# Kernel optimization log

Hardware: AMD Instinct MI355X
Metric: run time of the kernel (lower is better)

The kernel has to match this reference:

```python
import jax, jax.numpy as jnp
import numpy as np

EMSIZE = 1024
NHEAD = 16
HEAD = EMSIZE // NHEAD


def setup_inputs() -> dict:
    key = jax.random.key(0)
    ks = jax.random.split(key, 8)
    s = 1.0 / np.sqrt(EMSIZE)
    return {
        "embed": jax.random.normal(ks[0], (2, 2048, EMSIZE), dtype=jnp.float32),
        "q": jax.random.normal(ks[1], (2, 2048, EMSIZE), dtype=jnp.float32),
        "Wk": jax.random.normal(ks[2], (EMSIZE, EMSIZE), dtype=jnp.float32) * s,
        "bk": jnp.zeros((EMSIZE,), dtype=jnp.float32),
        "Wq": jax.random.normal(ks[3], (EMSIZE, EMSIZE), dtype=jnp.float32) * s,
        "bq": jnp.zeros((EMSIZE,), dtype=jnp.float32),
        "Wv": jax.random.normal(ks[4], (EMSIZE, EMSIZE), dtype=jnp.float32) * s,
        "bv": jnp.zeros((EMSIZE,), dtype=jnp.float32),
    }


def _split_heads(x):
    # [b, s, E] -> [b, h, s, d]
    b, s, _ = x.shape
    return x.reshape(b, s, NHEAD, HEAD).transpose(0, 2, 1, 3)


def reference(embed, q, Wk, bk, Wq, bq, Wv, bv):
    # torch Linear: y = x @ W.T + b
    k = _split_heads(embed @ Wk.T + bk)   # [b, h, skv, d]
    qh = _split_heads(q @ Wq.T + bq)      # [b, h, sq, d]
    v = _split_heads(embed @ Wv.T + bv)   # [b, h, skv, d]
    scale = 1.0 / np.sqrt(HEAD).astype(np.float32)
    scores = jnp.einsum("bhqd,bhkd->bhqk", qh, k) * scale
    attn = jax.nn.softmax(scores, axis=-1)  # dropout p=0 -> identity
    ctx = jnp.einsum("bhqk,bhkd->bhqd", attn, v)
    b, h, sq, d = ctx.shape
    return ctx.transpose(0, 2, 1, 3).reshape(b, sq, h * d)
```

## Files before the change

### kernel.cpp

```cpp
#include <hip/hip_runtime.h>
#include <cstdint>
#include <cstddef>


using bf16 = __bf16;
typedef __bf16 bf16x8 __attribute__((ext_vector_type(8)));
typedef float f32x4 __attribute__((ext_vector_type(4)));
typedef float f32x16 __attribute__((ext_vector_type(16)));
using uint32 = unsigned int;

__device__ __forceinline__ void async16(void* lds, const void* g) {
  __builtin_amdgcn_global_load_lds((__attribute__((address_space(1))) void*)g,
                                   (__attribute__((address_space(3))) void*)lds,
                                   16, 0, 0);
}

__device__ __forceinline__ uint32 pack_bf16x2(float lo, float hi_) {
  union { bf16 h[2]; uint32 u; } w;
  w.h[0] = (bf16)lo; w.h[1] = (bf16)hi_;
  return w.u;
}

__global__ void cast_all_kernel(const float* __restrict__ e, const float* __restrict__ q,
                                const float* __restrict__ wk, const float* __restrict__ wq,
                                const float* __restrict__ wv, bf16* __restrict__ dst) {
  int i = blockIdx.x * blockDim.x + threadIdx.x;
  if (i >= 2883584) return;
  const float* src; int off;
  if (i < 1048576)      { src = e;  off = 0; }
  else if (i < 2097152) { src = q;  off = 1048576; }
  else if (i < 2359296) { src = wk; off = 2097152; }
  else if (i < 2621440) { src = wq; off = 2359296; }
  else                  { src = wv; off = 2621440; }
  float4 v = reinterpret_cast<const float4*>(src)[i - off];
  union { bf16 h[4]; unsigned long long u; } o;
  o.h[0] = (bf16)v.x; o.h[1] = (bf16)v.y; o.h[2] = (bf16)v.z; o.h[3] = (bf16)v.w;
  reinterpret_cast<unsigned long long*>(dst)[i] = o.u;
}

__global__ __launch_bounds__(256) void proj_kernel(
    const bf16* __restrict__ emb, const bf16* __restrict__ qin,
    const bf16* __restrict__ wk, const bf16* __restrict__ wq, const bf16* __restrict__ wv,
    const float* __restrict__ bk, const float* __restrict__ bq, const float* __restrict__ bv,
    bf16* __restrict__ Kp, bf16* __restrict__ Qp, bf16* __restrict__ Vt)
{
  __shared__ bf16 As[128 * 64];
  __shared__ bf16 Bs[128 * 64];

  int pid = blockIdx.x;
  int proj = pid >> 8;
  int t = pid & 255;
  int m0 = (t >> 3) * 128;
  int n0 = (t & 7) * 128;

  const bf16* A = (proj == 1) ? qin : emb;
  const bf16* W = (proj == 0) ? wk : (proj == 1) ? wq : wv;
  const float* bias = (proj == 0) ? bk : (proj == 1) ? bq : bv;
  const bool proj2 = (proj == 2);

  int tid = threadIdx.x;
  int lane = tid & 63, wid = tid >> 6;
  int quad = lane >> 4, l16 = lane & 15;
  int moff = (wid & 1) * 64, noff = (wid >> 1) * 64;

  f32x4 zero = {0.f, 0.f, 0.f, 0.f};
  f32x4 acc[4][4];
#pragma unroll
  for (int i = 0; i < 4; i++)
#pragma unroll
    for (int j = 0; j < 4; j++) acc[i][j] = zero;

  for (int kk = 0; kk < 1024; kk += 64) {
    __syncthreads();
#pragma unroll
    for (int i = 0; i < 4; i++) {
      int c = i * 256 + tid;
      int row = c >> 3;
      int ko = ((c ^ row) & 7) << 3;
      async16(&As[(size_t)(i * 256 + wid * 64) * 8], &A[(size_t)(m0 + row) * 1024 + kk + ko]);
      async16(&Bs[(size_t)(i * 256 + wid * 64) * 8], &W[(size_t)(n0 + row) * 1024 + kk + ko]);
    }
    __syncthreads();
#pragma unroll
    for (int ks = 0; ks < 2; ks++) {
      bf16x8 af[4], bfr[4];
#pragma unroll
      for (int i = 0; i < 4; i++) {
        int row = moff + i * 16 + l16;
        af[i] = *reinterpret_cast<const bf16x8*>(&As[row * 64 + ((((ks << 2) | quad) ^ row) & 7) * 8]);
      }
#pragma unroll
      for (int j = 0; j < 4; j++) {
        int row = noff + j * 16 + l16;
        bfr[j] = *reinterpret_cast<const bf16x8*>(&Bs[row * 64 + ((((ks << 2) | quad) ^ row) & 7) * 8]);
      }
      if (proj2) {
#pragma unroll
        for (int i = 0; i < 4; i++)
#pragma unroll
          for (int j = 0; j < 4; j++)
            acc[i][j] = __builtin_amdgcn_mfma_f32_16x16x32_bf16(bfr[j], af[i], acc[i][j], 0, 0, 0);
      } else {
#pragma unroll
        for (int i = 0; i < 4; i++)
#pragma unroll
          for (int j = 0; j < 4; j++)
            acc[i][j] = __builtin_amdgcn_mfma_f32_16x16x32_bf16(af[i], bfr[j], acc[i][j], 0, 0, 0);
      }
    }
  }

  if (proj2) {
#pragma unroll
    for (int i = 0; i < 4; i++) {
      int grow = m0 + moff + i * 16 + l16;
      int bb = grow >> 11;
      int ss = grow & 2047;
#pragma unroll
      for (int j = 0; j < 4; j++) {
#pragma unroll
        for (int r = 0; r < 4; r++) {
          int gcol = n0 + noff + j * 16 + quad * 4 + r;
          int hh = gcol >> 6, dd = gcol & 63;
          int bh = bb * 16 + hh;
          float v = acc[i][j][r] + bias[gcol];
          Vt[((size_t)bh * 64 + dd) * 2048 + ss] = (bf16)v;
        }
      }
    }
  } else {
    float bvv[4];
#pragma unroll
    for (int j = 0; j < 4; j++) bvv[j] = bias[n0 + noff + j * 16 + l16];
    bf16* dst = (proj == 0) ? Kp : Qp;
    const float qs = (proj == 1) ? 0.18033688011112042f : 1.0f;
#pragma unroll
    for (int i = 0; i < 4; i++) {
#pragma unroll
      for (int r = 0; r < 4; r++) {
        int grow = m0 + moff + i * 16 + quad * 4 + r;
        int bb = grow >> 11;
        int ss = grow & 2047;
#pragma unroll
        for (int j = 0; j < 4; j++) {
          int gcol = n0 + noff + j * 16 + l16;
          int hh = gcol >> 6, dd = gcol & 63;
          int bh = bb * 16 + hh;
          float v = (acc[i][j][r] + bvv[j]) * qs;
          dst[((size_t)bh * 2048 + ss) * 64 + dd] = (bf16)v;
        }
      }
    }
  }
}

__global__ __launch_bounds__(256, 2) void attn_kernel(
    const bf16* __restrict__ Qp, const bf16* __restrict__ Kp, const bf16* __restrict__ Vt,
    float* __restrict__ out, float* __restrict__ part1, float* __restrict__ lbuf)
{
  __shared__ bf16 Ks[2][64 * 64];
  __shared__ bf16 Vs[2][64 * 64];

  int bid = blockIdx.x;
  int half = bid & 1;
  int q0 = ((bid >> 1) & 7) << 8;
  int bh = bid >> 4;
  int bb = bh >> 4, hh = bh & 15;
  int g0 = half << 4;

  const bf16* Qg = Qp + (size_t)bh * (2048 * 64);
  const bf16* Kg = Kp + (size_t)bh * (2048 * 64);
  const bf16* Vg = Vt + (size_t)bh * (64 * 2048);

  int tid = threadIdx.x, lane = tid & 63, wid = tid >> 6;
  int l32 = lane & 31;
  int h = lane >> 5;
  int wq0 = q0 + wid * 64;

  auto stage = [&](int kt_, int buf) {
#pragma unroll
    for (int i = 0; i < 2; i++) {
      int c = i * 256 + tid;
      int row = c >> 3;
      int srow = (row & ~12) | ((row & 4) << 1) | ((row & 8) >> 1);
      int ko = ((c ^ row) & 7) << 3;
      async16(&Ks[buf][(size_t)(i * 256 + wid * 64) * 8], &Kg[(size_t)(kt_ * 64 + srow) * 64 + ko]);
      async16(&Vs[buf][(size_t)(i * 256 + wid * 64) * 8], &Vg[(size_t)row * 2048 + kt_ * 64 + ko]);
    }
  };

  bf16x8 qf[2][4];
#pragma unroll
  for (int u = 0; u < 2; u++)
#pragma unroll
    for (int s = 0; s < 4; s++)
      qf[u][s] = *reinterpret_cast<const bf16x8*>(
          &Qg[(size_t)(wq0 + u * 32 + l32) * 64 + s * 16 + h * 8]);

  stage(g0, 0);

  const f32x16 z16 = {0.f, 0.f, 0.f, 0.f, 0.f, 0.f, 0.f, 0.f,
                      0.f, 0.f, 0.f, 0.f, 0.f, 0.f, 0.f, 0.f};
  f32x16 Ov[2][2];
  Ov[0][0] = z16; Ov[0][1] = z16; Ov[1][0] = z16; Ov[1][1] = z16;
  float l_i[2] = {0.f, 0.f};

  for (int kt = 0; kt < 16; kt++) {
    int cur = kt & 1;
    __syncthreads();
    __builtin_amdgcn_sched_barrier(0);
    if (kt < 15) stage(g0 + kt + 1, cur ^ 1);
    __builtin_amdgcn_sched_barrier(0);

    const bf16* Kc = Ks[cur];
    const bf16* Vc = Vs[cur];

#pragma unroll
    for (int t = 0; t < 2; t++) {
      f32x16 St[2];
      int row = t * 32 + l32;
      {
        bf16x8 kf = *reinterpret_cast<const bf16x8*>(&Kc[row * 64 + ((h ^ row) & 7) * 8]);
        St[0] = __builtin_amdgcn_mfma_f32_32x32x16_bf16(kf, qf[0][0], z16, 0, 0, 0);
        St[1] = __builtin_amdgcn_mfma_f32_32x32x16_bf16(kf, qf[1][0], z16, 0, 0, 0);
      }
#pragma unroll
      for (int s = 1; s < 4; s++) {
        int j8 = s * 2 + h;
        bf16x8 kf = *reinterpret_cast<const bf16x8*>(&Kc[row * 64 + ((j8 ^ row) & 7) * 8]);
        St[0] = __builtin_amdgcn_mfma_f32_32x32x16_bf16(kf, qf[0][s], St[0], 0, 0, 0);
        St[1] = __builtin_amdgcn_mfma_f32_32x32x16_bf16(kf, qf[1][s], St[1], 0, 0, 0);
      }

      uint32 pk[2][8];
#pragma unroll
      for (int u = 0; u < 2; u++) {
#pragma unroll
        for (int i = 0; i < 16; i++) {
          float p = __builtin_amdgcn_exp2f(St[u][i]);
          St[u][i] = p;
          l_i[u] += p;
        }
#pragma unroll
        for (int i = 0; i < 8; i++)
          pk[u][i] = pack_bf16x2(St[u][2 * i], St[u][2 * i + 1]);
      }

#pragma unroll
      for (int g = 0; g < 2; g++) {
        union { uint32 u[4]; bf16x8 v; } pb0, pb1;
#pragma unroll
        for (int i = 0; i < 4; i++) { pb0.u[i] = pk[0][g * 4 + i]; pb1.u[i] = pk[1][g * 4 + i]; }
        int j8 = t * 4 + g * 2 + h;
#pragma unroll
        for (int dt = 0; dt < 2; dt++) {
          int rowv = dt * 32 + l32;
          bf16x8 vf = *reinterpret_cast<const bf16x8*>(&Vc[rowv * 64 + ((j8 ^ rowv) & 7) * 8]);
          Ov[0][dt] = __builtin_amdgcn_mfma_f32_32x32x16_bf16(vf, pb0.v, Ov[0][dt], 0, 0, 0);
          Ov[1][dt] = __builtin_amdgcn_mfma_f32_32x32x16_bf16(vf, pb1.v, Ov[1][dt], 0, 0, 0);
        }
      }
    }
  }

#pragma unroll
  for (int u = 0; u < 2; u++) {
    float l_tot = l_i[u] + __shfl_xor(l_i[u], 32);
    int q = wq0 + u * 32 + l32;
    float* dstO = (half == 0 ? out : part1) + ((size_t)bb * 2048 + q) * 1024 + hh * 64;
#pragma unroll
    for (int dt = 0; dt < 2; dt++)
#pragma unroll
      for (int g = 0; g < 4; g++) {
        float4 o;
        o.x = Ov[u][dt][4 * g + 0];
        o.y = Ov[u][dt][4 * g + 1];
        o.z = Ov[u][dt][4 * g + 2];
        o.w = Ov[u][dt][4 * g + 3];
        *reinterpret_cast<float4*>(&dstO[dt * 32 + g * 8 + 4 * h]) = o;
      }
    if (h == 0) lbuf[half * 65536 + (bh << 11) + q] = l_tot;
  }
}

__global__ __launch_bounds__(256) void combine_kernel(
    float* __restrict__ out, const float* __restrict__ part1,
    const float* __restrict__ lbuf) {
  int i = blockIdx.x * 256 + threadIdx.x;
  int e = i << 2;
  int brow = e >> 10;
  int b = brow >> 11;
  int hcol = (e >> 6) & 15;
  int srow = brow & 2047;
  int lidx = ((b * 16 + hcol) << 11) + srow;
  float inv = 1.0f / (lbuf[lidx] + lbuf[65536 + lidx]);
  float4 a = reinterpret_cast<const float4*>(out)[i];
  float4 p = reinterpret_cast<const float4*>(part1)[i];
  float4 r;
  r.x = (a.x + p.x) * inv;
  r.y = (a.y + p.y) * inv;
  r.z = (a.z + p.z) * inv;
  r.w = (a.w + p.w) * inv;
  reinterpret_cast<float4*>(out)[i] = r;
}

extern "C" void kernel_launch(void* const* d_in, const int* in_sizes, int n_in,
                              void* d_out, int out_size, void* d_ws, size_t ws_size,
                              hipStream_t stream) {
  (void)in_sizes; (void)n_in; (void)out_size; (void)ws_size;
  const float* embed = (const float*)d_in[0];
  const float* qin   = (const float*)d_in[1];
  const float* Wk    = (const float*)d_in[2];
  const float* bk    = (const float*)d_in[3];
  const float* Wq    = (const float*)d_in[4];
  const float* bq    = (const float*)d_in[5];
  const float* Wv    = (const float*)d_in[6];
  const float* bv    = (const float*)d_in[7];
  float* out = (float*)d_out;

  bf16* ws = (bf16*)d_ws;
  bf16* emb_bf = ws;
  bf16* q_bf   = emb_bf + 4194304;
  bf16* wk_bf  = q_bf   + 4194304;
  bf16* wq_bf  = wk_bf  + 1048576;
  bf16* wv_bf  = wq_bf  + 1048576;
  bf16* Kp     = wv_bf  + 1048576;
  bf16* Qp     = Kp     + 4194304;
  bf16* Vt     = Qp     + 4194304;

  float* part1 = (float*)d_ws;
  float* lbuf  = part1 + 4194304;

  cast_all_kernel<<<11264, 256, 0, stream>>>(embed, qin, Wk, Wq, Wv, ws);

  proj_kernel<<<768, 256, 0, stream>>>(emb_bf, q_bf, wk_bf, wq_bf, wv_bf,
                                       bk, bq, bv, Kp, Qp, Vt);
  attn_kernel<<<512, 256, 0, stream>>>(Qp, Kp, Vt, out, part1, lbuf);
  combine_kernel<<<4096, 256, 0, stream>>>(out, part1, lbuf);
}
```

Baseline: 193.6 us.

## Restructure attention inner loop: batch K loads, compute all QK scores, prioritize MFMA phases

Reorders the per-tile attention loop so that all K fragments are loaded from LDS first and both QK^T score blocks are computed back to back. V fragments are then loaded ahead of each softmax/PV phase. s_setprio raises wave priority around the MFMA bursts so that different waves' matrix and exp work interleave better. The row-sum accumulator is split into two independent partial sums to shorten the dependency chain. In exchange, more fragments are held in registers at once (all K fragments plus both score tiles), which raises VGPR pressure and may lower occupancy.

```diff
diff --git a/kernel.cpp b/kernel.cpp
--- a/kernel.cpp
+++ b/kernel.cpp
@@ -203,7 +203,8 @@
                       0.f, 0.f, 0.f, 0.f, 0.f, 0.f, 0.f, 0.f};
   f32x16 Ov[2][2];
   Ov[0][0] = z16; Ov[0][1] = z16; Ov[1][0] = z16; Ov[1][1] = z16;
-  float l_i[2] = {0.f, 0.f};
+  float2 l2[2];
+  l2[0].x = 0.f; l2[0].y = 0.f; l2[1].x = 0.f; l2[1].y = 0.f;
 
   for (int kt = 0; kt < 16; kt++) {
     int cur = kt & 1;
@@ -215,57 +216,110 @@
     const bf16* Kc = Ks[cur];
     const bf16* Vc = Vs[cur];
 
+    bf16x8 kf[2][4];
 #pragma unroll
     for (int t = 0; t < 2; t++) {
-      f32x16 St[2];
       int row = t * 32 + l32;
-      {
-        bf16x8 kf = *reinterpret_cast<const bf16x8*>(&Kc[row * 64 + ((h ^ row) & 7) * 8]);
-        St[0] = __builtin_amdgcn_mfma_f32_32x32x16_bf16(kf, qf[0][0], z16, 0, 0, 0);
-        St[1] = __builtin_amdgcn_mfma_f32_32x32x16_bf16(kf, qf[1][0], z16, 0, 0, 0);
-      }
+#pragma unroll
+      for (int s = 0; s < 4; s++) {
+        int j8 = s * 2 + h;
+        kf[t][s] = *reinterpret_cast<const bf16x8*>(&Kc[row * 64 + ((j8 ^ row) & 7) * 8]);
+      }
+    }
+
+    f32x16 St[2][2];
+    __builtin_amdgcn_s_setprio(1);
+#pragma unroll
+    for (int t = 0; t < 2; t++) {
+      St[t][0] = __builtin_amdgcn_mfma_f32_32x32x16_bf16(kf[t][0], qf[0][0], z16, 0, 0, 0);
+      St[t][1] = __builtin_amdgcn_mfma_f32_32x32x16_bf16(kf[t][0], qf[1][0], z16, 0, 0, 0);
 #pragma unroll
       for (int s = 1; s < 4; s++) {
-        int j8 = s * 2 + h;
-        bf16x8 kf = *reinterpret_cast<const bf16x8*>(&Kc[row * 64 + ((j8 ^ row) & 7) * 8]);
-        St[0] = __builtin_amdgcn_mfma_f32_32x32x16_bf16(kf, qf[0][s], St[0], 0, 0, 0);
-        St[1] = __builtin_amdgcn_mfma_f32_32x32x16_bf16(kf, qf[1][s], St[1], 0, 0, 0);
-      }
-
-      uint32 pk[2][8];
-#pragma unroll
-      for (int u = 0; u < 2; u++) {
-#pragma unroll
-        for (int i = 0; i < 16; i++) {
-          float p = __builtin_amdgcn_exp2f(St[u][i]);
-          St[u][i] = p;
-          l_i[u] += p;
-        }
-#pragma unroll
-        for (int i = 0; i < 8; i++)
-          pk[u][i] = pack_bf16x2(St[u][2 * i], St[u][2 * i + 1]);
-      }
-
-#pragma unroll
-      for (int g = 0; g < 2; g++) {
-        union { uint32 u[4]; bf16x8 v; } pb0, pb1;
-#pragma unroll
-        for (int i = 0; i < 4; i++) { pb0.u[i] = pk[0][g * 4 + i]; pb1.u[i] = pk[1][g * 4 + i]; }
-        int j8 = t * 4 + g * 2 + h;
-#pragma unroll
-        for (int dt = 0; dt < 2; dt++) {
-          int rowv = dt * 32 + l32;
-          bf16x8 vf = *reinterpret_cast<const bf16x8*>(&Vc[rowv * 64 + ((j8 ^ rowv) & 7) * 8]);
-          Ov[0][dt] = __builtin_amdgcn_mfma_f32_32x32x16_bf16(vf, pb0.v, Ov[0][dt], 0, 0, 0);
-          Ov[1][dt] = __builtin_amdgcn_mfma_f32_32x32x16_bf16(vf, pb1.v, Ov[1][dt], 0, 0, 0);
-        }
-      }
-    }
+        St[t][0] = __builtin_amdgcn_mfma_f32_32x32x16_bf16(kf[t][s], qf[0][s], St[t][0], 0, 0, 0);
+        St[t][1] = __builtin_amdgcn_mfma_f32_32x32x16_bf16(kf[t][s], qf[1][s], St[t][1], 0, 0, 0);
+      }
+    }
+    __builtin_amdgcn_s_setprio(0);
+
+    bf16x8 vf0[2][2];
+#pragma unroll
+    for (int g = 0; g < 2; g++) {
+      int j8 = g * 2 + h;
+#pragma unroll
+      for (int dt = 0; dt < 2; dt++) {
+        int rowv = dt * 32 + l32;
+        vf0[g][dt] = *reinterpret_cast<const bf16x8*>(&Vc[rowv * 64 + ((j8 ^ rowv) & 7) * 8]);
+      }
+    }
+
+    uint32 pk0[2][8];
+#pragma unroll
+    for (int u = 0; u < 2; u++) {
+#pragma unroll
+      for (int i = 0; i < 8; i++) {
+        float pe = __builtin_amdgcn_exp2f(St[0][u][2 * i]);
+        float po = __builtin_amdgcn_exp2f(St[0][u][2 * i + 1]);
+        l2[u].x += pe; l2[u].y += po;
+        pk0[u][i] = pack_bf16x2(pe, po);
+      }
+    }
+
+    __builtin_amdgcn_s_setprio(1);
+#pragma unroll
+    for (int g = 0; g < 2; g++) {
+      union { uint32 u[4]; bf16x8 v; } pb0, pb1;
+#pragma unroll
+      for (int i = 0; i < 4; i++) { pb0.u[i] = pk0[0][g * 4 + i]; pb1.u[i] = pk0[1][g * 4 + i]; }
+#pragma unroll
+      for (int dt = 0; dt < 2; dt++) {
+        Ov[0][dt] = __builtin_amdgcn_mfma_f32_32x32x16_bf16(vf0[g][dt], pb0.v, Ov[0][dt], 0, 0, 0);
+        Ov[1][dt] = __builtin_amdgcn_mfma_f32_32x32x16_bf16(vf0[g][dt], pb1.v, Ov[1][dt], 0, 0, 0);
+      }
+    }
+    __builtin_amdgcn_s_setprio(0);
+
+    bf16x8 vf1[2][2];
+#pragma unroll
+    for (int g = 0; g < 2; g++) {
+      int j8 = 4 + g * 2 + h;
+#pragma unroll
+      for (int dt = 0; dt < 2; dt++) {
+        int rowv = dt * 32 + l32;
+        vf1[g][dt] = *reinterpret_cast<const bf16x8*>(&Vc[rowv * 64 + ((j8 ^ rowv) & 7) * 8]);
+      }
+    }
+
+    uint32 pk1[2][8];
+#pragma unroll
+    for (int u = 0; u < 2; u++) {
+#pragma unroll
+      for (int i = 0; i < 8; i++) {
+        float pe = __builtin_amdgcn_exp2f(St[1][u][2 * i]);
+        float po = __builtin_amdgcn_exp2f(St[1][u][2 * i + 1]);
+        l2[u].x += pe; l2[u].y += po;
+        pk1[u][i] = pack_bf16x2(pe, po);
+      }
+    }
+
+    __builtin_amdgcn_s_setprio(1);
+#pragma unroll
+    for (int g = 0; g < 2; g++) {
+      union { uint32 u[4]; bf16x8 v; } pb0, pb1;
+#pragma unroll
+      for (int i = 0; i < 4; i++) { pb0.u[i] = pk1[0][g * 4 + i]; pb1.u[i] = pk1[1][g * 4 + i]; }
+#pragma unroll
+      for (int dt = 0; dt < 2; dt++) {
+        Ov[0][dt] = __builtin_amdgcn_mfma_f32_32x32x16_bf16(vf1[g][dt], pb0.v, Ov[0][dt], 0, 0, 0);
+        Ov[1][dt] = __builtin_amdgcn_mfma_f32_32x32x16_bf16(vf1[g][dt], pb1.v, Ov[1][dt], 0, 0, 0);
+      }
+    }
+    __builtin_amdgcn_s_setprio(0);
   }
 
 #pragma unroll
   for (int u = 0; u < 2; u++) {
-    float l_tot = l_i[u] + __shfl_xor(l_i[u], 32);
+    float l_half = l2[u].x + l2[u].y;
+    float l_tot = l_half + __shfl_xor(l_half, 32);
     int q = wq0 + u * 32 + l32;
     float* dstO = (half == 0 ? out : part1) + ((size_t)bb * 2048 + q) * 1024 + hh * 64;
 #pragma unroll
```

Result: no change. 196.2 us (+1.3%).

## Split attention work across 8 waves with 32 query rows each

Applied to the files above, without the earlier changes.

The attention kernel now launches 512 threads per block, and each wave handles 32 query rows instead of 64. This halves the per-wave accumulators and Q fragments so more waves can be resident (launch bounds 512,4). K/V staging now takes one async load per thread instead of two. Each K/V fragment read from LDS now feeds one MFMA instead of two, so there is less register-level reuse and more LDS traffic per MFMA.

```diff
diff --git a/kernel.cpp b/kernel.cpp
--- a/kernel.cpp
+++ b/kernel.cpp
@@ -154,7 +154,7 @@
   }
 }
 
-__global__ __launch_bounds__(256, 2) void attn_kernel(
+__global__ __launch_bounds__(512, 4) void attn_kernel(
     const bf16* __restrict__ Qp, const bf16* __restrict__ Kp, const bf16* __restrict__ Vt,
     float* __restrict__ out, float* __restrict__ part1, float* __restrict__ lbuf)
 {
@@ -175,35 +175,31 @@
   int tid = threadIdx.x, lane = tid & 63, wid = tid >> 6;
   int l32 = lane & 31;
   int h = lane >> 5;
-  int wq0 = q0 + wid * 64;
+  int wq0 = q0 + wid * 32;
 
   auto stage = [&](int kt_, int buf) {
-#pragma unroll
-    for (int i = 0; i < 2; i++) {
-      int c = i * 256 + tid;
-      int row = c >> 3;
-      int srow = (row & ~12) | ((row & 4) << 1) | ((row & 8) >> 1);
-      int ko = ((c ^ row) & 7) << 3;
-      async16(&Ks[buf][(size_t)(i * 256 + wid * 64) * 8], &Kg[(size_t)(kt_ * 64 + srow) * 64 + ko]);
-      async16(&Vs[buf][(size_t)(i * 256 + wid * 64) * 8], &Vg[(size_t)row * 2048 + kt_ * 64 + ko]);
-    }
+    int c = tid;
+    int row = c >> 3;
+    int srow = (row & ~12) | ((row & 4) << 1) | ((row & 8) >> 1);
+    int ko = ((c ^ row) & 7) << 3;
+    async16(&Ks[buf][(size_t)(wid * 64) * 8], &Kg[(size_t)(kt_ * 64 + srow) * 64 + ko]);
+    async16(&Vs[buf][(size_t)(wid * 64) * 8], &Vg[(size_t)row * 2048 + kt_ * 64 + ko]);
   };
 
-  bf16x8 qf[2][4];
-#pragma unroll
-  for (int u = 0; u < 2; u++)
-#pragma unroll
-    for (int s = 0; s < 4; s++)
-      qf[u][s] = *reinterpret_cast<const bf16x8*>(
-          &Qg[(size_t)(wq0 + u * 32 + l32) * 64 + s * 16 + h * 8]);
+  bf16x8 qf[4];
+#pragma unroll
+  for (int s = 0; s < 4; s++)
+    qf[s] = *reinterpret_cast<const bf16x8*>(
+        &Qg[(size_t)(wq0 + l32) * 64 + s * 16 + h * 8]);
 
   stage(g0, 0);
 
   const f32x16 z16 = {0.f, 0.f, 0.f, 0.f, 0.f, 0.f, 0.f, 0.f,
                       0.f, 0.f, 0.f, 0.f, 0.f, 0.f, 0.f, 0.f};
-  f32x16 Ov[2][2];
-  Ov[0][0] = z16; Ov[0][1] = z16; Ov[1][0] = z16; Ov[1][1] = z16;
-  float l_i[2] = {0.f, 0.f};
+  f32x16 Ov[2];
+  Ov[0] = z16; Ov[1] = z16;
+  float2 l2;
+  l2.x = 0.f; l2.y = 0.f;
 
   for (int kt = 0; kt < 16; kt++) {
     int cur = kt & 1;
@@ -217,66 +213,58 @@
 
 #pragma unroll
     for (int t = 0; t < 2; t++) {
-      f32x16 St[2];
+      f32x16 St;
       int row = t * 32 + l32;
       {
         bf16x8 kf = *reinterpret_cast<const bf16x8*>(&Kc[row * 64 + ((h ^ row) & 7) * 8]);
-        St[0] = __builtin_amdgcn_mfma_f32_32x32x16_bf16(kf, qf[0][0], z16, 0, 0, 0);
-        St[1] = __builtin_amdgcn_mfma_f32_32x32x16_bf16(kf, qf[1][0], z16, 0, 0, 0);
+        St = __builtin_amdgcn_mfma_f32_32x32x16_bf16(kf, qf[0], z16, 0, 0, 0);
       }
 #pragma unroll
       for (int s = 1; s < 4; s++) {
         int j8 = s * 2 + h;
         bf16x8 kf = *reinterpret_cast<const bf16x8*>(&Kc[row * 64 + ((j8 ^ row) & 7) * 8]);
-        St[0] = __builtin_amdgcn_mfma_f32_32x32x16_bf16(kf, qf[0][s], St[0], 0, 0, 0);
-        St[1] = __builtin_amdgcn_mfma_f32_32x32x16_bf16(kf, qf[1][s], St[1], 0, 0, 0);
-      }
-
-      uint32 pk[2][8];
-#pragma unroll
-      for (int u = 0; u < 2; u++) {
-#pragma unroll
-        for (int i = 0; i < 16; i++) {
-          float p = __builtin_amdgcn_exp2f(St[u][i]);
-          St[u][i] = p;
-          l_i[u] += p;
-        }
-#pragma unroll
-        for (int i = 0; i < 8; i++)
-          pk[u][i] = pack_bf16x2(St[u][2 * i], St[u][2 * i + 1]);
+        St = __builtin_amdgcn_mfma_f32_32x32x16_bf16(kf, qf[s], St, 0, 0, 0);
+      }
+
+      uint32 pk[8];
+#pragma unroll
+      for (int i = 0; i < 8; i++) {
+        float pe = __builtin_amdgcn_exp2f(St[2 * i]);
+        float po = __builtin_amdgcn_exp2f(St[2 * i + 1]);
+        l2.x += pe; l2.y += po;
+        pk[i] = pack_bf16x2(pe, po);
       }
 
 #pragma unroll
       for (int g = 0; g < 2; g++) {
-        union { uint32 u[4]; bf16x8 v; } pb0, pb1;
-#pragma unroll
-        for (int i = 0; i < 4; i++) { pb0.u[i] = pk[0][g * 4 + i]; pb1.u[i] = pk[1][g * 4 + i]; }
+        union { uint32 u[4]; bf16x8 v; } pb;
+#pragma unroll
+        for (int i = 0; i < 4; i++) pb.u[i] = pk[g * 4 + i];
         int j8 = t * 4 + g * 2 + h;
 #pragma unroll
         for (int dt = 0; dt < 2; dt++) {
           int rowv = dt * 32 + l32;
           bf16x8 vf = *reinterpret_cast<const bf16x8*>(&Vc[rowv * 64 + ((j8 ^ rowv) & 7) * 8]);
-          Ov[0][dt] = __builtin_amdgcn_mfma_f32_32x32x16_bf16(vf, pb0.v, Ov[0][dt], 0, 0, 0);
-          Ov[1][dt] = __builtin_amdgcn_mfma_f32_32x32x16_bf16(vf, pb1.v, Ov[1][dt], 0, 0, 0);
+          Ov[dt] = __builtin_amdgcn_mfma_f32_32x32x16_bf16(vf, pb.v, Ov[dt], 0, 0, 0);
         }
       }
     }
   }
 
-#pragma unroll
-  for (int u = 0; u < 2; u++) {
-    float l_tot = l_i[u] + __shfl_xor(l_i[u], 32);
-    int q = wq0 + u * 32 + l32;
+  {
+    float l_half = l2.x + l2.y;
+    float l_tot = l_half + __shfl_xor(l_half, 32);
+    int q = wq0 + l32;
     float* dstO = (half == 0 ? out : part1) + ((size_t)bb * 2048 + q) * 1024 + hh * 64;
 #pragma unroll
     for (int dt = 0; dt < 2; dt++)
 #pragma unroll
       for (int g = 0; g < 4; g++) {
         float4 o;
-        o.x = Ov[u][dt][4 * g + 0];
-        o.y = Ov[u][dt][4 * g + 1];
-        o.z = Ov[u][dt][4 * g + 2];
-        o.w = Ov[u][dt][4 * g + 3];
+        o.x = Ov[dt][4 * g + 0];
+        o.y = Ov[dt][4 * g + 1];
+        o.z = Ov[dt][4 * g + 2];
+        o.w = Ov[dt][4 * g + 3];
         *reinterpret_cast<float4*>(&dstO[dt * 32 + g * 8 + 4 * h]) = o;
       }
     if (h == 0) lbuf[half * 65536 + (bh << 11) + q] = l_tot;
@@ -335,6 +323,6 @@
 
   proj_kernel<<<768, 256, 0, stream>>>(emb_bf, q_bf, wk_bf, wq_bf, wv_bf,
                                        bk, bq, bv, Kp, Qp, Vt);
-  attn_kernel<<<512, 256, 0, stream>>>(Qp, Kp, Vt, out, part1, lbuf);
+  attn_kernel<<<512, 512, 0, stream>>>(Qp, Kp, Vt, out, part1, lbuf);
   combine_kernel<<<4096, 256, 0, stream>>>(out, part1, lbuf);
 }
```

New measurement: 192.5 us. About the same (-0.6%).

## Split KV across waves within block and reduce in LDS, drop combine kernel

Applied to the files above, without the earlier changes.

The attention kernel now uses 512-thread blocks, each covering 128 query rows. Eight waves split the key sequence four ways (two 64-key tiles per stage and two 32-row halves), and the partial outputs and row sums are reduced through shared memory at the end. This removes the separate combine kernel and the global round trip of partial outputs and sums, and adds a block-index swizzle. In exchange it adds more LDS traffic and extra barriers in the epilogue, and needs more registers per block.

```diff
diff --git a/kernel.cpp b/kernel.cpp
--- a/kernel.cpp
+++ b/kernel.cpp
@@ -154,19 +154,19 @@
   }
 }
 
-__global__ __launch_bounds__(256, 2) void attn_kernel(
+__global__ __launch_bounds__(512, 4) void attn_kernel(
     const bf16* __restrict__ Qp, const bf16* __restrict__ Kp, const bf16* __restrict__ Vt,
-    float* __restrict__ out, float* __restrict__ part1, float* __restrict__ lbuf)
+    float* __restrict__ out)
 {
-  __shared__ bf16 Ks[2][64 * 64];
-  __shared__ bf16 Vs[2][64 * 64];
-
-  int bid = blockIdx.x;
-  int half = bid & 1;
-  int q0 = ((bid >> 1) & 7) << 8;
-  int bh = bid >> 4;
+  __shared__ bf16 Ks[2][2][64 * 64];
+  __shared__ bf16 Vs[2][2][64 * 64];
+  __shared__ float lsh[4][128];
+
+  int swz = (blockIdx.x & 7) * 64 + (blockIdx.x >> 3);
+  int qblk = swz & 15;
+  int bh = swz >> 4;
+  int q0 = qblk << 7;
   int bb = bh >> 4, hh = bh & 15;
-  int g0 = half << 4;
 
   const bf16* Qg = Qp + (size_t)bh * (2048 * 64);
   const bf16* Kg = Kp + (size_t)bh * (2048 * 64);
@@ -175,17 +175,21 @@
   int tid = threadIdx.x, lane = tid & 63, wid = tid >> 6;
   int l32 = lane & 31;
   int h = lane >> 5;
-  int wq0 = q0 + wid * 64;
-
-  auto stage = [&](int kt_, int buf) {
-#pragma unroll
-    for (int i = 0; i < 2; i++) {
-      int c = i * 256 + tid;
+  int qh = wid & 1;
+  int kh = (wid >> 1) & 1;
+  int ts = wid >> 2;
+  int wq0 = q0 + qh * 64;
+
+  auto stage = [&](int kp_, int buf) {
+#pragma unroll
+    for (int s = 0; s < 2; s++) {
+      int kt_ = kp_ * 2 + s;
+      int c = tid;
       int row = c >> 3;
       int srow = (row & ~12) | ((row & 4) << 1) | ((row & 8) >> 1);
       int ko = ((c ^ row) & 7) << 3;
-      async16(&Ks[buf][(size_t)(i * 256 + wid * 64) * 8], &Kg[(size_t)(kt_ * 64 + srow) * 64 + ko]);
-      async16(&Vs[buf][(size_t)(i * 256 + wid * 64) * 8], &Vg[(size_t)row * 2048 + kt_ * 64 + ko]);
+      async16(&Ks[buf][s][(size_t)wid * 512], &Kg[(size_t)(kt_ * 64 + srow) * 64 + ko]);
+      async16(&Vs[buf][s][(size_t)wid * 512], &Vg[(size_t)row * 2048 + kt_ * 64 + ko]);
     }
   };
 
@@ -197,111 +201,165 @@
       qf[u][s] = *reinterpret_cast<const bf16x8*>(
           &Qg[(size_t)(wq0 + u * 32 + l32) * 64 + s * 16 + h * 8]);
 
-  stage(g0, 0);
+  stage(0, 0);
 
   const f32x16 z16 = {0.f, 0.f, 0.f, 0.f, 0.f, 0.f, 0.f, 0.f,
                       0.f, 0.f, 0.f, 0.f, 0.f, 0.f, 0.f, 0.f};
   f32x16 Ov[2][2];
   Ov[0][0] = z16; Ov[0][1] = z16; Ov[1][0] = z16; Ov[1][1] = z16;
-  float l_i[2] = {0.f, 0.f};
-
-  for (int kt = 0; kt < 16; kt++) {
-    int cur = kt & 1;
+  float2 l2[2];
+  l2[0].x = 0.f; l2[0].y = 0.f; l2[1].x = 0.f; l2[1].y = 0.f;
+
+  int row = kh * 32 + l32;
+
+  for (int kp = 0; kp < 16; kp++) {
+    int cur = kp & 1;
     __syncthreads();
     __builtin_amdgcn_sched_barrier(0);
-    if (kt < 15) stage(g0 + kt + 1, cur ^ 1);
+    if (kp < 15) stage(kp + 1, cur ^ 1);
     __builtin_amdgcn_sched_barrier(0);
 
-    const bf16* Kc = Ks[cur];
-    const bf16* Vc = Vs[cur];
-
-#pragma unroll
-    for (int t = 0; t < 2; t++) {
-      f32x16 St[2];
-      int row = t * 32 + l32;
-      {
-        bf16x8 kf = *reinterpret_cast<const bf16x8*>(&Kc[row * 64 + ((h ^ row) & 7) * 8]);
-        St[0] = __builtin_amdgcn_mfma_f32_32x32x16_bf16(kf, qf[0][0], z16, 0, 0, 0);
-        St[1] = __builtin_amdgcn_mfma_f32_32x32x16_bf16(kf, qf[1][0], z16, 0, 0, 0);
-      }
-#pragma unroll
-      for (int s = 1; s < 4; s++) {
-        int j8 = s * 2 + h;
-        bf16x8 kf = *reinterpret_cast<const bf16x8*>(&Kc[row * 64 + ((j8 ^ row) & 7) * 8]);
-        St[0] = __builtin_amdgcn_mfma_f32_32x32x16_bf16(kf, qf[0][s], St[0], 0, 0, 0);
-        St[1] = __builtin_amdgcn_mfma_f32_32x32x16_bf16(kf, qf[1][s], St[1], 0, 0, 0);
-      }
-
-      uint32 pk[2][8];
-#pragma unroll
-      for (int u = 0; u < 2; u++) {
-#pragma unroll
-        for (int i = 0; i < 16; i++) {
-          float p = __builtin_amdgcn_exp2f(St[u][i]);
-          St[u][i] = p;
-          l_i[u] += p;
-        }
-#pragma unroll
-        for (int i = 0; i < 8; i++)
-          pk[u][i] = pack_bf16x2(St[u][2 * i], St[u][2 * i + 1]);
-      }
-
-#pragma unroll
-      for (int g = 0; g < 2; g++) {
-        union { uint32 u[4]; bf16x8 v; } pb0, pb1;
-#pragma unroll
-        for (int i = 0; i < 4; i++) { pb0.u[i] = pk[0][g * 4 + i]; pb1.u[i] = pk[1][g * 4 + i]; }
-        int j8 = t * 4 + g * 2 + h;
-#pragma unroll
-        for (int dt = 0; dt < 2; dt++) {
-          int rowv = dt * 32 + l32;
-          bf16x8 vf = *reinterpret_cast<const bf16x8*>(&Vc[rowv * 64 + ((j8 ^ rowv) & 7) * 8]);
-          Ov[0][dt] = __builtin_amdgcn_mfma_f32_32x32x16_bf16(vf, pb0.v, Ov[0][dt], 0, 0, 0);
-          Ov[1][dt] = __builtin_amdgcn_mfma_f32_32x32x16_bf16(vf, pb1.v, Ov[1][dt], 0, 0, 0);
-        }
-      }
-    }
-  }
-
-#pragma unroll
-  for (int u = 0; u < 2; u++) {
-    float l_tot = l_i[u] + __shfl_xor(l_i[u], 32);
-    int q = wq0 + u * 32 + l32;
-    float* dstO = (half == 0 ? out : part1) + ((size_t)bb * 2048 + q) * 1024 + hh * 64;
-#pragma unroll
-    for (int dt = 0; dt < 2; dt++)
-#pragma unroll
-      for (int g = 0; g < 4; g++) {
-        float4 o;
-        o.x = Ov[u][dt][4 * g + 0];
-        o.y = Ov[u][dt][4 * g + 1];
-        o.z = Ov[u][dt][4 * g + 2];
-        o.w = Ov[u][dt][4 * g + 3];
-        *reinterpret_cast<float4*>(&dstO[dt * 32 + g * 8 + 4 * h]) = o;
-      }
-    if (h == 0) lbuf[half * 65536 + (bh << 11) + q] = l_tot;
-  }
-}
-
-__global__ __launch_bounds__(256) void combine_kernel(
-    float* __restrict__ out, const float* __restrict__ part1,
-    const float* __restrict__ lbuf) {
-  int i = blockIdx.x * 256 + threadIdx.x;
-  int e = i << 2;
-  int brow = e >> 10;
-  int b = brow >> 11;
-  int hcol = (e >> 6) & 15;
-  int srow = brow & 2047;
-  int lidx = ((b * 16 + hcol) << 11) + srow;
-  float inv = 1.0f / (lbuf[lidx] + lbuf[65536 + lidx]);
-  float4 a = reinterpret_cast<const float4*>(out)[i];
-  float4 p = reinterpret_cast<const float4*>(part1)[i];
-  float4 r;
-  r.x = (a.x + p.x) * inv;
-  r.y = (a.y + p.y) * inv;
-  r.z = (a.z + p.z) * inv;
-  r.w = (a.w + p.w) * inv;
-  reinterpret_cast<float4*>(out)[i] = r;
+    const bf16* Kc = Ks[cur][ts];
+    const bf16* Vc = Vs[cur][ts];
+
+    f32x16 St[2];
+    {
+      bf16x8 kf = *reinterpret_cast<const bf16x8*>(&Kc[row * 64 + ((h ^ row) & 7) * 8]);
+      St[0] = __builtin_amdgcn_mfma_f32_32x32x16_bf16(kf, qf[0][0], z16, 0, 0, 0);
+      St[1] = __builtin_amdgcn_mfma_f32_32x32x16_bf16(kf, qf[1][0], z16, 0, 0, 0);
+    }
+#pragma unroll
+    for (int s = 1; s < 4; s++) {
+      int j8 = s * 2 + h;
+      bf16x8 kf = *reinterpret_cast<const bf16x8*>(&Kc[row * 64 + ((j8 ^ row) & 7) * 8]);
+      St[0] = __builtin_amdgcn_mfma_f32_32x32x16_bf16(kf, qf[0][s], St[0], 0, 0, 0);
+      St[1] = __builtin_amdgcn_mfma_f32_32x32x16_bf16(kf, qf[1][s], St[1], 0, 0, 0);
+    }
+
+    uint32 pk[2][8];
+#pragma unroll
+    for (int u = 0; u < 2; u++) {
+#pragma unroll
+      for (int i = 0; i < 8; i++) {
+        float pe = __builtin_amdgcn_exp2f(St[u][2 * i]);
+        float po = __builtin_amdgcn_exp2f(St[u][2 * i + 1]);
+        l2[u].x += pe; l2[u].y += po;
+        pk[u][i] = pack_bf16x2(pe, po);
+      }
+    }
+
+#pragma unroll
+    for (int g = 0; g < 2; g++) {
+      union { uint32 u[4]; bf16x8 v; } pb0, pb1;
+#pragma unroll
+      for (int i = 0; i < 4; i++) { pb0.u[i] = pk[0][g * 4 + i]; pb1.u[i] = pk[1][g * 4 + i]; }
+      int j8 = kh * 4 + g * 2 + h;
+#pragma unroll
+      for (int dt = 0; dt < 2; dt++) {
+        int rowv = dt * 32 + l32;
+        bf16x8 vf = *reinterpret_cast<const bf16x8*>(&Vc[rowv * 64 + ((j8 ^ rowv) & 7) * 8]);
+        Ov[0][dt] = __builtin_amdgcn_mfma_f32_32x32x16_bf16(vf, pb0.v, Ov[0][dt], 0, 0, 0);
+        Ov[1][dt] = __builtin_amdgcn_mfma_f32_32x32x16_bf16(vf, pb1.v, Ov[1][dt], 0, 0, 0);
+      }
+    }
+  }
+
+  {
+    int grp = kh * 2 + ts;
+#pragma unroll
+    for (int u = 0; u < 2; u++) {
+      float s = l2[u].x + l2[u].y;
+      s += __shfl_xor(s, 32);
+      if (h == 0) lsh[grp][qh * 64 + u * 32 + l32] = s;
+    }
+  }
+
+  auto region = [&](int r) -> float* {
+    return (r < 2) ? (reinterpret_cast<float*>(&Ks[0][0][0]) + r * 4096)
+                   : (reinterpret_cast<float*>(&Vs[0][0][0]) + (r - 2) * 4096);
+  };
+
+  __syncthreads();
+  if (ts == 1) {
+    float* dst = region(qh * 2 + kh);
+#pragma unroll
+    for (int u = 0; u < 2; u++)
+#pragma unroll
+      for (int dt = 0; dt < 2; dt++)
+#pragma unroll
+        for (int g = 0; g < 4; g++) {
+          float4 o;
+          o.x = Ov[u][dt][4 * g + 0];
+          o.y = Ov[u][dt][4 * g + 1];
+          o.z = Ov[u][dt][4 * g + 2];
+          o.w = Ov[u][dt][4 * g + 3];
+          *reinterpret_cast<float4*>(&dst[(((u * 2 + dt) * 4 + g) * 64 + lane) * 4]) = o;
+        }
+  }
+  __syncthreads();
+  if (ts == 0) {
+    const float* src = region(qh * 2 + kh);
+#pragma unroll
+    for (int u = 0; u < 2; u++)
+#pragma unroll
+      for (int dt = 0; dt < 2; dt++)
+#pragma unroll
+        for (int g = 0; g < 4; g++) {
+          float4 a = *reinterpret_cast<const float4*>(&src[(((u * 2 + dt) * 4 + g) * 64 + lane) * 4]);
+          Ov[u][dt][4 * g + 0] += a.x; Ov[u][dt][4 * g + 1] += a.y;
+          Ov[u][dt][4 * g + 2] += a.z; Ov[u][dt][4 * g + 3] += a.w;
+        }
+  }
+  __syncthreads();
+  if (ts == 0 && kh == 1) {
+    float* dst = region(qh);
+#pragma unroll
+    for (int u = 0; u < 2; u++)
+#pragma unroll
+      for (int dt = 0; dt < 2; dt++)
+#pragma unroll
+        for (int g = 0; g < 4; g++) {
+          float4 o;
+          o.x = Ov[u][dt][4 * g + 0];
+          o.y = Ov[u][dt][4 * g + 1];
+          o.z = Ov[u][dt][4 * g + 2];
+          o.w = Ov[u][dt][4 * g + 3];
+          *reinterpret_cast<float4*>(&dst[(((u * 2 + dt) * 4 + g) * 64 + lane) * 4]) = o;
+        }
+  }
+  __syncthreads();
+  if (ts == 0 && kh == 0) {
+    const float* src = region(qh);
+#pragma unroll
+    for (int u = 0; u < 2; u++)
+#pragma unroll
+      for (int dt = 0; dt < 2; dt++)
+#pragma unroll
+        for (int g = 0; g < 4; g++) {
+          float4 a = *reinterpret_cast<const float4*>(&src[(((u * 2 + dt) * 4 + g) * 64 + lane) * 4]);
+          Ov[u][dt][4 * g + 0] += a.x; Ov[u][dt][4 * g + 1] += a.y;
+          Ov[u][dt][4 * g + 2] += a.z; Ov[u][dt][4 * g + 3] += a.w;
+        }
+#pragma unroll
+    for (int u = 0; u < 2; u++) {
+      int ql = qh * 64 + u * 32 + l32;
+      float l_tot = lsh[0][ql] + lsh[1][ql] + lsh[2][ql] + lsh[3][ql];
+      float inv = 1.0f / l_tot;
+      int q = wq0 + u * 32 + l32;
+      float* dstO = out + ((size_t)bb * 2048 + q) * 1024 + hh * 64;
+#pragma unroll
+      for (int dt = 0; dt < 2; dt++)
+#pragma unroll
+        for (int g = 0; g < 4; g++) {
+          float4 o;
+          o.x = Ov[u][dt][4 * g + 0] * inv;
+          o.y = Ov[u][dt][4 * g + 1] * inv;
+          o.z = Ov[u][dt][4 * g + 2] * inv;
+          o.w = Ov[u][dt][4 * g + 3] * inv;
+          *reinterpret_cast<float4*>(&dstO[dt * 32 + g * 8 + 4 * h]) = o;
+        }
+    }
+  }
 }
 
 extern "C" void kernel_launch(void* const* d_in, const int* in_sizes, int n_in,
@@ -328,13 +386,9 @@
   bf16* Qp     = Kp     + 4194304;
   bf16* Vt     = Qp     + 4194304;
 
-  float* part1 = (float*)d_ws;
-  float* lbuf  = part1 + 4194304;
-
   cast_all_kernel<<<11264, 256, 0, stream>>>(embed, qin, Wk, Wq, Wv, ws);
 
   proj_kernel<<<768, 256, 0, stream>>>(emb_bf, q_bf, wk_bf, wq_bf, wv_bf,
                                        bk, bq, bv, Kp, Qp, Vt);
-  attn_kernel<<<512, 256, 0, stream>>>(Qp, Kp, Vt, out, part1, lbuf);
-  combine_kernel<<<4096, 256, 0, stream>>>(out, part1, lbuf);
-}
+  attn_kernel<<<512, 512, 0, stream>>>(Qp, Kp, Vt, out);
+}
```

Result: slower. 230.0 us (+18.8%).
